# Performance work log

Hardware: AMD Instinct MI355X
Metric: run time of the kernel (lower is better)

The kernel has to match this reference:

```python
import jax, jax.numpy as jnp
import numpy as np

ONE_STEP = 14
EPS = 1e-5


def _bn(x, g, b):
    # training-mode batchnorm over the node/batch axis (biased variance)
    m = jnp.mean(x, axis=0)
    v = jnp.var(x, axis=0)
    return (x - m) * jax.lax.rsqrt(v + EPS) * g + b


def _gcn_conv(x, W, b, src, dst, dis):
    N = x.shape[0]
    h = x @ W
    norm = (dis[src] * dis[dst])[:, None]
    agg = jax.ops.segment_sum(h[src] * norm, dst, num_segments=N)
    agg = agg + (dis * dis)[:, None] * h  # self-loop contribution
    return agg + b


def setup_inputs() -> dict:
    key = jax.random.key(0)
    ks = jax.random.split(key, 16)
    N, F, E, NC = 114688, 512, 917504, 10
    x = jax.random.normal(ks[0], (N, F), jnp.float32)
    edge_index = jax.random.randint(ks[1], (2, E), 0, N, jnp.int32)

    def lin(k, i, o):
        return jax.random.normal(k, (i, o), jnp.float32) / np.sqrt(i).astype(np.float32)

    d = {"x": x, "edge_index": edge_index}
    dims = [(F, 128), (128, 256), (256, 64), (64, 32)]
    for li, (i, o) in enumerate(dims, 1):
        d[f"W{li}"] = lin(ks[1 + li], i, o)
        d[f"b{li}"] = jnp.zeros((o,), jnp.float32)
        d[f"bn{li}_g"] = jnp.ones((o,), jnp.float32)
        d[f"bn{li}_b"] = jnp.zeros((o,), jnp.float32)
    d["gW1"] = lin(ks[6], 32, 16); d["gb1"] = jnp.zeros((16,), jnp.float32)
    d["gbn1_g"] = jnp.ones((16,), jnp.float32); d["gbn1_b"] = jnp.zeros((16,), jnp.float32)
    d["gW2"] = lin(ks[7], 16, 1); d["gb2"] = jnp.zeros((1,), jnp.float32)
    d["gbn2_g"] = jnp.ones((1,), jnp.float32); d["gbn2_b"] = jnp.zeros((1,), jnp.float32)
    d["fcW"] = lin(ks[8], 32, NC); d["fcb"] = jnp.zeros((NC,), jnp.float32)
    return d


def reference(x, edge_index, W1, b1, bn1_g, bn1_b, W2, b2, bn2_g, bn2_b,
              W3, b3, bn3_g, bn3_b, W4, b4, bn4_g, bn4_b,
              gW1, gb1, gbn1_g, gbn1_b, gW2, gb2, gbn2_g, gbn2_b, fcW, fcb):
    N = x.shape[0]
    src, dst = edge_index[0], edge_index[1]
    # degree with self-loops (counted on dst, per PyG gcn_norm)
    deg = jax.ops.segment_sum(jnp.ones_like(dst, jnp.float32), dst, num_segments=N) + 1.0
    dis = jax.lax.rsqrt(deg)

    h = _bn(jax.nn.relu(_gcn_conv(x, W1, b1, src, dst, dis)), bn1_g, bn1_b)
    h = _bn(jax.nn.relu(_gcn_conv(h, W2, b2, src, dst, dis)), bn2_g, bn2_b)
    h = _bn(jax.nn.relu(_gcn_conv(h, W3, b3, src, dst, dis)), bn3_g, bn3_b)
    h = _bn(jax.nn.relu(_gcn_conv(h, W4, b4, src, dst, dis)), bn4_g, bn4_b)

    # gate network: Linear -> BN -> ReLU -> Linear -> BN -> ReLU
    g = jax.nn.relu(_bn(h @ gW1 + gb1, gbn1_g, gbn1_b))
    g = jax.nn.relu(_bn(g @ gW2 + gb2, gbn2_g, gbn2_b))[:, 0]  # [N]

    B = N // ONE_STEP
    batch = jnp.repeat(jnp.arange(B), ONE_STEP)
    # segment softmax over nodes of each graph
    m = jax.ops.segment_max(g, batch, num_segments=B)
    e = jnp.exp(g - m[batch])
    s = jax.ops.segment_sum(e, batch, num_segments=B)
    alpha = e / s[batch]
    pooled = jax.ops.segment_sum(alpha[:, None] * h, batch, num_segments=B)  # [B,32]

    # dropout is identity in eval mode
    logits = pooled @ fcW + fcb
    return jax.nn.softmax(logits, axis=1)
```

## Files before the change

kernel.cpp:

```cpp
#include <hip/hip_runtime.h>

#define NN 114688
#define NE 917504
#define NBATCH 8192
#define GSZ 14
#define NCLS 10
#define EPSB 1e-5f
#define NSCAN 112

typedef unsigned short u16;
typedef short bf16x8 __attribute__((ext_vector_type(8)));
typedef float f32x4 __attribute__((ext_vector_type(4)));
typedef _Float16 h8t __attribute__((ext_vector_type(8)));
typedef unsigned short u16x8 __attribute__((ext_vector_type(8)));

__device__ __forceinline__ float bf2f(u16 u) {
    union { unsigned int i; float f; } v; v.i = ((unsigned int)u) << 16; return v.f;
}
__device__ __forceinline__ u16 f2bf(float f) {
    union { float f; unsigned int i; } v; v.f = f;
    unsigned int i = v.i;
    unsigned int r = i + 0x7FFFu + ((i >> 16) & 1u);
    return (u16)(r >> 16);
}
__device__ __forceinline__ void splitbf(float y, u16& h, u16& l) {
    h = f2bf(y);
    l = f2bf(y - bf2f(h));
}

__global__ __launch_bounds__(256) void k_hist(const int* __restrict__ ei, int* __restrict__ counts) {
    int e = blockIdx.x * 256 + threadIdx.x;
    atomicAdd(&counts[ei[NE + e]], 1);
}

__global__ __launch_bounds__(256) void k_scan1(const int* __restrict__ counts, int* __restrict__ bsum) {
    __shared__ int red[256];
    int tid = threadIdx.x;
    int base = blockIdx.x * 1024 + tid * 4;
    int s = counts[base] + counts[base + 1] + counts[base + 2] + counts[base + 3];
    red[tid] = s; __syncthreads();
    for (int o = 128; o > 0; o >>= 1) {
        if (tid < o) red[tid] += red[tid + o];
        __syncthreads();
    }
    if (tid == 0) bsum[blockIdx.x] = red[0];
}

__global__ void k_scan2(int* bsum, int* offs) {
    if (threadIdx.x == 0) {
        int run = 0;
        for (int i = 0; i < NSCAN; i++) { int t = bsum[i]; bsum[i] = run; run += t; }
        offs[NN] = run;
    }
}

__global__ __launch_bounds__(256) void k_scan3(const int* __restrict__ counts, const int* __restrict__ bsum,
                                               int* __restrict__ offs) {
    __shared__ int ss[256];
    int tid = threadIdx.x;
    int base = blockIdx.x * 1024 + tid * 4;
    int v0 = counts[base], v1 = counts[base + 1], v2 = counts[base + 2], v3 = counts[base + 3];
    int ts = v0 + v1 + v2 + v3;
    ss[tid] = ts; __syncthreads();
    for (int o = 1; o < 256; o <<= 1) {
        int add = (tid >= o) ? ss[tid - o] : 0;
        __syncthreads();
        ss[tid] += add;
        __syncthreads();
    }
    int excl = ss[tid] - ts + bsum[blockIdx.x];
    offs[base] = excl;
    offs[base + 1] = excl + v0;
    offs[base + 2] = excl + v0 + v1;
    offs[base + 3] = excl + v0 + v1 + v2;
}

__global__ __launch_bounds__(256) void k_dis_cursor(const int* __restrict__ counts, const int* __restrict__ offs,
                                                    float* __restrict__ dis, int* __restrict__ cursor) {
    int n = blockIdx.x * 256 + threadIdx.x;
    dis[n] = rsqrtf((float)counts[n] + 1.0f);
    cursor[n] = offs[n];
}

__global__ __launch_bounds__(256) void k_scatter(const int* __restrict__ ei, int* __restrict__ cursor,
                                                 int* __restrict__ srcs, float* __restrict__ sd,
                                                 const float* __restrict__ dis, float* __restrict__ wsa) {
    int e = blockIdx.x * 256 + threadIdx.x;
    int d = ei[NE + e], s = ei[e];
    int p = atomicAdd(&cursor[d], 1);
    float w = dis[s];
    srcs[p] = s;
    sd[p] = w;
    atomicAdd(&wsa[d], w);
}

__global__ __launch_bounds__(256) void k_tsplit(const float* __restrict__ Wsrc,
                                                u16* __restrict__ Wh, u16* __restrict__ Wl,
                                                int K, int F) {
    int i = blockIdx.x * 256 + threadIdx.x;
    if (i < K * F) {
        int k = i / F, f = i % F;
        u16 h, l; splitbf(Wsrc[i], h, l);
        Wh[f * K + k] = h;
        Wl[f * K + k] = l;
    }
}

__global__ __launch_bounds__(256) void k_wsplit(const float* __restrict__ W, const float* __restrict__ sc,
                                                u16* __restrict__ Wh, u16* __restrict__ Wl,
                                                int K, int F) {
    int i = blockIdx.x * 256 + threadIdx.x;
    if (i < K * F) {
        int k = i / F, f = i % F;
        u16 h, l; splitbf(sc[k] * W[i], h, l);
        Wh[f * K + k] = h;
        Wl[f * K + k] = l;
    }
}

__global__ __launch_bounds__(256) void k_wc2(const float* __restrict__ W, const float* __restrict__ sh,
                                             float* __restrict__ c2, int K, int F) {
    int wv = (blockIdx.x * 256 + threadIdx.x) >> 6;
    int lane = threadIdx.x & 63;
    if (wv >= F) return;
    float acc = 0.f;
    for (int k = lane; k < K; k += 64) acc += sh[k] * W[k * F + wv];
#pragma unroll
    for (int o = 1; o < 64; o <<= 1) acc += __shfl_xor(acc, o);
    if (lane == 0) c2[wv] = acc;
}

template<int BM, int BN, int WCOLS, bool AFP32, bool C2, bool TEPI>
__global__ __launch_bounds__(256) void k_gemm(
    const float* __restrict__ Af, const u16* __restrict__ Ahi, const u16* __restrict__ Alo,
    const u16* __restrict__ Wh, const u16* __restrict__ Wl,
    _Float16* __restrict__ C, const int K, const int Fout, const float* __restrict__ c2,
    const float* __restrict__ bias, const float* __restrict__ wsa, const float* __restrict__ disv,
    u16* __restrict__ Thi, u16* __restrict__ Tlo, float* __restrict__ Sg, float* __restrict__ Qg)
{
    constexpr int AST = 40;
    __shared__ u16 Ah[BM][AST], Al[BM][AST];
    __shared__ u16 Bh[BN][AST], Bl[BN][AST];
    __shared__ float redS[TEPI ? BN : 1], redQ[TEPI ? BN : 1];

    const int tid = threadIdx.x;
    const int row0 = blockIdx.y * BM;
    const int col0 = blockIdx.x * BN;

    const int wave = tid >> 6, lane = tid & 63;
    const int mb = (wave / WCOLS) * 64;
    const int nb = (wave % WCOLS) * 64;
    const int lm = lane & 15;
    const int lk = (lane >> 4) * 8;
    const int cb = col0 + nb + lm;

    if constexpr (TEPI) {
        for (int i = tid; i < BN; i += 256) { redS[i] = 0.f; redQ[i] = 0.f; }
    }

    float c2v[4] = {0.f, 0.f, 0.f, 0.f};
    if constexpr (C2) {
#pragma unroll
        for (int ni = 0; ni < 4; ni++) c2v[ni] = c2[cb + ni * 16];
    }

    f32x4 acc[4][4];
#pragma unroll
    for (int i = 0; i < 4; i++)
#pragma unroll
        for (int j = 0; j < 4; j++)
#pragma unroll
            for (int r = 0; r < 4; r++) acc[i][j][r] = c2v[j];

    const int stg_r = tid >> 3;
    const int stg_c = (tid & 7) * 4;

    for (int k0 = 0; k0 < K; k0 += 32) {
        __syncthreads();
#pragma unroll
        for (int p = 0; p < BM / 32; p++) {
            const int r = p * 32 + stg_r;
            if constexpr (AFP32) {
                const float4 v = *(const float4*)(Af + (size_t)(row0 + r) * K + k0 + stg_c);
                float y[4] = {v.x, v.y, v.z, v.w};
                ushort4 hv, lv;
#pragma unroll
                for (int q = 0; q < 4; q++) splitbf(y[q], ((u16*)&hv)[q], ((u16*)&lv)[q]);
                *(ushort4*)&Ah[r][stg_c] = hv;
                *(ushort4*)&Al[r][stg_c] = lv;
            } else {
                *(ushort4*)&Ah[r][stg_c] = *(const ushort4*)(Ahi + (size_t)(row0 + r) * K + k0 + stg_c);
                *(ushort4*)&Al[r][stg_c] = *(const ushort4*)(Alo + (size_t)(row0 + r) * K + k0 + stg_c);
            }
        }
#pragma unroll
        for (int p = 0; p < BN / 32; p++) {
            const int n = p * 32 + stg_r;
            *(ushort4*)&Bh[n][stg_c] = *(const ushort4*)(Wh + (size_t)(col0 + n) * K + k0 + stg_c);
            *(ushort4*)&Bl[n][stg_c] = *(const ushort4*)(Wl + (size_t)(col0 + n) * K + k0 + stg_c);
        }
        __syncthreads();

        bf16x8 ah[4], al[4], bh[4], bl[4];
#pragma unroll
        for (int mi = 0; mi < 4; mi++) {
            ah[mi] = *(const bf16x8*)&Ah[mb + mi * 16 + lm][lk];
            al[mi] = *(const bf16x8*)&Al[mb + mi * 16 + lm][lk];
        }
#pragma unroll
        for (int ni = 0; ni < 4; ni++) {
            bh[ni] = *(const bf16x8*)&Bh[nb + ni * 16 + lm][lk];
            bl[ni] = *(const bf16x8*)&Bl[nb + ni * 16 + lm][lk];
        }
#pragma unroll
        for (int mi = 0; mi < 4; mi++)
#pragma unroll
            for (int ni = 0; ni < 4; ni++) {
                acc[mi][ni] = __builtin_amdgcn_mfma_f32_16x16x32_bf16(al[mi], bh[ni], acc[mi][ni], 0, 0, 0);
                acc[mi][ni] = __builtin_amdgcn_mfma_f32_16x16x32_bf16(ah[mi], bl[ni], acc[mi][ni], 0, 0, 0);
                acc[mi][ni] = __builtin_amdgcn_mfma_f32_16x16x32_bf16(ah[mi], bh[ni], acc[mi][ni], 0, 0, 0);
            }
    }

    const int rb = row0 + mb + (lane >> 4) * 4;
    if constexpr (TEPI) {
        float c2l[4], bl4[4];
#pragma unroll
        for (int ni = 0; ni < 4; ni++) { c2l[ni] = c2[cb + ni * 16]; bl4[ni] = bias[cb + ni * 16]; }
        float ws[4][4];
#pragma unroll
        for (int mi = 0; mi < 4; mi++)
#pragma unroll
            for (int r = 0; r < 4; r++) {
                const int row = rb + mi * 16 + r;
                const float d = disv[row];
                ws[mi][r] = d * wsa[row] + d * d;
            }
#pragma unroll
        for (int ni = 0; ni < 4; ni++) {
            float s = 0.f, q = 0.f;
#pragma unroll
            for (int mi = 0; mi < 4; mi++)
#pragma unroll
                for (int r = 0; r < 4; r++) {
                    float v = acc[mi][ni][r] + ws[mi][r] * c2l[ni] + bl4[ni];
                    v = fmaxf(v, 0.f);
                    s += v; q += v * v;
                    u16 hh, ll; splitbf(v, hh, ll);
                    const size_t idx = (size_t)(rb + mi * 16 + r) * Fout + cb + ni * 16;
                    Thi[idx] = hh;
                    Tlo[idx] = ll;
                }
            atomicAdd(&redS[nb + ni * 16 + lm], s);
            atomicAdd(&redQ[nb + ni * 16 + lm], q);
        }
        __syncthreads();
        for (int i = tid; i < BN; i += 256) {
            atomicAdd(&Sg[col0 + i], redS[i]);
            atomicAdd(&Qg[col0 + i], redQ[i]);
        }
    } else {
#pragma unroll
        for (int mi = 0; mi < 4; mi++)
#pragma unroll
            for (int ni = 0; ni < 4; ni++)
#pragma unroll
                for (int r = 0; r < 4; r++)
                    C[(size_t)(rb + mi * 16 + r) * Fout + cb + ni * 16] = (_Float16)acc[mi][ni][r];
    }
}

template<int CH, bool FP16OUT>
__global__ __launch_bounds__(256) void k_agg(
    const _Float16* __restrict__ h, u16* __restrict__ thi, u16* __restrict__ tlo,
    const float* __restrict__ bias,
    const int* __restrict__ off, const int* __restrict__ srcs, const float* __restrict__ sd,
    const float* __restrict__ dis, float* __restrict__ statS, float* __restrict__ statQ,
    _Float16* __restrict__ tf)
{
    constexpr int ECH = 16;
    constexpr int LPG = CH / ECH;
    constexpr int NSUB = 64 / LPG;
    __shared__ float redS[CH], redQ[CH];
    const int tid = threadIdx.x;
    for (int i = tid; i < CH; i += 256) { redS[i] = 0.f; redQ[i] = 0.f; }
    __syncthreads();

    const int lane = tid & 63;
    const int sub = lane / LPG;
    const int c = (lane % LPG) * ECH;
    const int wid = (blockIdx.x * 256 + tid) >> 6;
    const int nw = (gridDim.x * 256) >> 6;

    float bs[ECH], bq[ECH], bv[ECH];
#pragma unroll
    for (int v = 0; v < ECH; v++) { bs[v] = 0.f; bq[v] = 0.f; bv[v] = bias[c + v]; }

    for (int n = wid; n < NN; n += nw) {
        const int p0 = off[n], p1 = off[n + 1];
        float a[ECH];
#pragma unroll
        for (int v = 0; v < ECH; v++) a[v] = 0.f;

        int p = p0 + sub;
        int s = 0; float w = 0.f;
        if (p < p1) { s = srcs[p]; w = sd[p]; }
        while (p < p1) {
            const int pn = p + NSUB;
            int s2 = 0; float w2 = 0.f;
            if (pn < p1) { s2 = srcs[pn]; w2 = sd[pn]; }
            const _Float16* hr = h + (size_t)s * CH + c;
            h8t hv0 = *(const h8t*)hr;
            h8t hv1 = *(const h8t*)(hr + 8);
#pragma unroll
            for (int v = 0; v < 8; v++) { a[v] += w * (float)hv0[v]; a[v + 8] += w * (float)hv1[v]; }
            s = s2; w = w2; p = pn;
        }
#pragma unroll
        for (int o = LPG; o < 64; o <<= 1) {
#pragma unroll
            for (int v = 0; v < ECH; v++) a[v] += __shfl_xor(a[v], o);
        }
        if (sub == 0) {
            const float dn = dis[n];
            const float dn2 = dn * dn;
            const _Float16* hr = h + (size_t)n * CH + c;
            h8t hn0 = *(const h8t*)hr;
            h8t hn1 = *(const h8t*)(hr + 8);
            float o16[ECH];
#pragma unroll
            for (int v = 0; v < 8; v++) {
                o16[v] = fmaxf(dn * a[v] + dn2 * (float)hn0[v] + bv[v], 0.f);
                o16[v + 8] = fmaxf(dn * a[v + 8] + dn2 * (float)hn1[v] + bv[v + 8], 0.f);
            }
#pragma unroll
            for (int v = 0; v < ECH; v++) { bs[v] += o16[v]; bq[v] += o16[v] * o16[v]; }
            if constexpr (FP16OUT) {
                h8t o0, o1;
#pragma unroll
                for (int v = 0; v < 8; v++) { o0[v] = (_Float16)o16[v]; o1[v] = (_Float16)o16[v + 8]; }
                _Float16* tr = tf + (size_t)n * CH + c;
                *(h8t*)tr = o0; *(h8t*)(tr + 8) = o1;
            } else {
                u16x8 hv0, lv0, hv1, lv1;
#pragma unroll
                for (int v = 0; v < 8; v++) {
                    splitbf(o16[v], ((u16*)&hv0)[v], ((u16*)&lv0)[v]);
                    splitbf(o16[v + 8], ((u16*)&hv1)[v], ((u16*)&lv1)[v]);
                }
                u16* th = thi + (size_t)n * CH + c;
                u16* tl = tlo + (size_t)n * CH + c;
                *(u16x8*)th = hv0; *(u16x8*)(th + 8) = hv1;
                *(u16x8*)tl = lv0; *(u16x8*)(tl + 8) = lv1;
            }
        }
    }
    if (sub == 0) {
#pragma unroll
        for (int v = 0; v < ECH; v++) { atomicAdd(&redS[c + v], bs[v]); atomicAdd(&redQ[c + v], bq[v]); }
    }
    __syncthreads();
    for (int i = tid; i < CH; i += 256) { atomicAdd(&statS[i], redS[i]); atomicAdd(&statQ[i], redQ[i]); }
}

template<int CH>
__global__ __launch_bounds__(256) void k_agglin(
    const _Float16* __restrict__ t, u16* __restrict__ uhi, u16* __restrict__ ulo,
    const int* __restrict__ off, const int* __restrict__ srcs, const float* __restrict__ sd,
    const float* __restrict__ dis)
{
    constexpr int ECH = 16;
    constexpr int LPG = CH / ECH;
    constexpr int NSUB = 64 / LPG;
    const int tid = threadIdx.x;
    const int lane = tid & 63;
    const int sub = lane / LPG;
    const int c = (lane % LPG) * ECH;
    const int wid = (blockIdx.x * 256 + tid) >> 6;
    const int nw = (gridDim.x * 256) >> 6;

    for (int n = wid; n < NN; n += nw) {
        const int p0 = off[n], p1 = off[n + 1];
        float a[ECH];
#pragma unroll
        for (int v = 0; v < ECH; v++) a[v] = 0.f;

        int p = p0 + sub;
        int s = 0; float w = 0.f;
        if (p < p1) { s = srcs[p]; w = sd[p]; }
        while (p < p1) {
            const int pn = p + NSUB;
            int s2 = 0; float w2 = 0.f;
            if (pn < p1) { s2 = srcs[pn]; w2 = sd[pn]; }
            const _Float16* hr = t + (size_t)s * CH + c;
            h8t hv0 = *(const h8t*)hr;
            h8t hv1 = *(const h8t*)(hr + 8);
#pragma unroll
            for (int v = 0; v < 8; v++) { a[v] += w * (float)hv0[v]; a[v + 8] += w * (float)hv1[v]; }
            s = s2; w = w2; p = pn;
        }
#pragma unroll
        for (int o = LPG; o < 64; o <<= 1) {
#pragma unroll
            for (int v = 0; v < ECH; v++) a[v] += __shfl_xor(a[v], o);
        }
        if (sub == 0) {
            const float dn = dis[n];
            const float dn2 = dn * dn;
            const _Float16* hr = t + (size_t)n * CH + c;
            h8t hn0 = *(const h8t*)hr;
            h8t hn1 = *(const h8t*)(hr + 8);
            u16x8 hv0, lv0, hv1, lv1;
#pragma unroll
            for (int v = 0; v < 8; v++) {
                float o0 = dn * a[v] + dn2 * (float)hn0[v];
                float o1 = dn * a[v + 8] + dn2 * (float)hn1[v];
                splitbf(o0, ((u16*)&hv0)[v], ((u16*)&lv0)[v]);
                splitbf(o1, ((u16*)&hv1)[v], ((u16*)&lv1)[v]);
            }
            u16* th = uhi + (size_t)n * CH + c;
            u16* tl = ulo + (size_t)n * CH + c;
            *(u16x8*)th = hv0; *(u16x8*)(th + 8) = hv1;
            *(u16x8*)tl = lv0; *(u16x8*)(tl + 8) = lv1;
        }
    }
}

__global__ void k_bnpar(const float* __restrict__ S, const float* __restrict__ Q,
                        const float* __restrict__ g, const float* __restrict__ b,
                        float* __restrict__ sc, float* __restrict__ sh, int F) {
    int c = threadIdx.x;
    if (c >= F) return;
    const float invn = 1.0f / (float)NN;
    float mean = S[c] * invn;
    float var = Q[c] * invn - mean * mean;
    float s = g[c] * rsqrtf(fmaxf(var, 0.f) + EPSB);
    sc[c] = s;
    sh[c] = b[c] - mean * s;
}

template<int K, int F, bool BIAS, bool STATS>
__global__ __launch_bounds__(256) void k_smm(
    const u16* __restrict__ Ahi, const u16* __restrict__ Alo,
    const float* __restrict__ Wf, const float* __restrict__ bias,
    _Float16* __restrict__ C, const float* __restrict__ sc, const float* __restrict__ sh,
    float* __restrict__ Sg, float* __restrict__ Qg)
{
    __shared__ float Wl[K * F];
    __shared__ float scl[K], shl[K], bl[F];
    __shared__ float redS[F], redQ[F];
    const int tid = threadIdx.x;
    for (int i = tid; i < K * F; i += 256) Wl[i] = Wf[i];
    if (tid < K) { scl[tid] = sc[tid]; shl[tid] = sh[tid]; }
    if (tid < F) {
        bl[tid] = 0.f;
        if constexpr (BIAS) bl[tid] = bias[tid];
        if constexpr (STATS) { redS[tid] = 0.f; redQ[tid] = 0.f; }
    }
    __syncthreads();
    const int n = blockIdx.x * 256 + tid;
    float acc[F];
#pragma unroll
    for (int f = 0; f < F; f++) acc[f] = bl[f];
    const u16* ah = Ahi + (size_t)n * K;
    const u16* al = Alo + (size_t)n * K;
    for (int k = 0; k < K; k += 4) {
        ushort4 hv = *(const ushort4*)(ah + k);
        ushort4 lv = *(const ushort4*)(al + k);
        float y0 = (bf2f(hv.x) + bf2f(lv.x)) * scl[k] + shl[k];
        float y1 = (bf2f(hv.y) + bf2f(lv.y)) * scl[k + 1] + shl[k + 1];
        float y2 = (bf2f(hv.z) + bf2f(lv.z)) * scl[k + 2] + shl[k + 2];
        float y3 = (bf2f(hv.w) + bf2f(lv.w)) * scl[k + 3] + shl[k + 3];
#pragma unroll
        for (int f = 0; f < F; f += 4) {
            float4 w0 = *(const float4*)&Wl[k * F + f];
            float4 w1 = *(const float4*)&Wl[(k + 1) * F + f];
            float4 w2 = *(const float4*)&Wl[(k + 2) * F + f];
            float4 w3 = *(const float4*)&Wl[(k + 3) * F + f];
            acc[f + 0] += y0 * w0.x + y1 * w1.x + y2 * w2.x + y3 * w3.x;
            acc[f + 1] += y0 * w0.y + y1 * w1.y + y2 * w2.y + y3 * w3.y;
            acc[f + 2] += y0 * w0.z + y1 * w1.z + y2 * w2.z + y3 * w3.z;
            acc[f + 3] += y0 * w0.w + y1 * w1.w + y2 * w2.w + y3 * w3.w;
        }
    }
    _Float16* cr = C + (size_t)n * F;
#pragma unroll
    for (int f = 0; f < F; f++) cr[f] = (_Float16)acc[f];
    if constexpr (STATS) {
        float s[F], q[F];
#pragma unroll
        for (int f = 0; f < F; f++) { s[f] = acc[f]; q[f] = acc[f] * acc[f]; }
#pragma unroll
        for (int o = 1; o < 64; o <<= 1) {
#pragma unroll
            for (int f = 0; f < F; f++) { s[f] += __shfl_xor(s[f], o); q[f] += __shfl_xor(q[f], o); }
        }
        if ((tid & 63) == 0) {
#pragma unroll
            for (int f = 0; f < F; f++) { atomicAdd(&redS[f], s[f]); atomicAdd(&redQ[f], q[f]); }
        }
        __syncthreads();
        for (int i = tid; i < F; i += 256) { atomicAdd(&Sg[i], redS[i]); atomicAdd(&Qg[i], redQ[i]); }
    }
}

__global__ __launch_bounds__(256) void k_gate2(const _Float16* __restrict__ g1,
                                               const float* __restrict__ sc, const float* __restrict__ sh,
                                               const float* __restrict__ w2, const float* __restrict__ b2,
                                               float* __restrict__ g2,
                                               float* __restrict__ Sg, float* __restrict__ Qg) {
    __shared__ float wl[16], scl[16], shl[16], b2l[1];
    __shared__ float redSg[1], redQg[1];
    const int tid = threadIdx.x;
    if (tid < 16) { wl[tid] = w2[tid]; scl[tid] = sc[tid]; shl[tid] = sh[tid]; }
    if (tid == 0) { b2l[0] = b2[0]; redSg[0] = 0.f; redQg[0] = 0.f; }
    __syncthreads();
    const int n = blockIdx.x * 256 + tid;
    const _Float16* r = g1 + (size_t)n * 16;
    float acc = b2l[0];
#pragma unroll
    for (int k = 0; k < 16; k++) {
        float y = fmaxf((float)r[k] * scl[k] + shl[k], 0.f);
        acc += y * wl[k];
    }
    g2[n] = acc;
    float s = acc, q = acc * acc;
#pragma unroll
    for (int o = 1; o < 64; o <<= 1) { s += __shfl_xor(s, o); q += __shfl_xor(q, o); }
    if ((tid & 63) == 0) { atomicAdd(&redSg[0], s); atomicAdd(&redQg[0], q); }
    __syncthreads();
    if (tid == 0) { atomicAdd(&Sg[0], redSg[0]); atomicAdd(&Qg[0], redQg[0]); }
}

__global__ __launch_bounds__(256) void k_pool(const u16* __restrict__ t4hi, const u16* __restrict__ t4lo,
                                              const float* __restrict__ sc4, const float* __restrict__ sh4,
                                              const float* __restrict__ g2,
                                              const float* __restrict__ gsc2, const float* __restrict__ gsh2,
                                              const float* __restrict__ fcW, const float* __restrict__ fcb,
                                              float* __restrict__ out) {
    __shared__ float fw[32 * NCLS], fbl[NCLS], sc4l[32], sh4l[32];
    const int tid = threadIdx.x;
    for (int i = tid; i < 32 * NCLS; i += 256) fw[i] = fcW[i];
    if (tid < NCLS) fbl[tid] = fcb[tid];
    if (tid < 32) { sc4l[tid] = sc4[tid]; sh4l[tid] = sh4[tid]; }
    __syncthreads();
    const int b = blockIdx.x * 256 + tid;
    const float s2 = gsc2[0], h2 = gsh2[0];
    const int base = b * GSZ;

    float gv[GSZ];
    float m = -1e30f;
#pragma unroll
    for (int i = 0; i < GSZ; i++) {
        float v = fmaxf(g2[base + i] * s2 + h2, 0.f);
        gv[i] = v; m = fmaxf(m, v);
    }
    float ssum = 0.f;
#pragma unroll
    for (int i = 0; i < GSZ; i++) { float e = __expf(gv[i] - m); gv[i] = e; ssum += e; }
    const float inv = 1.0f / ssum;

    float pooled[32];
#pragma unroll
    for (int c = 0; c < 32; c++) pooled[c] = 0.f;
#pragma unroll
    for (int i = 0; i < GSZ; i++) {
        const float a = gv[i] * inv;
        const u16* th = t4hi + (size_t)(base + i) * 32;
        const u16* tl = t4lo + (size_t)(base + i) * 32;
#pragma unroll
        for (int c = 0; c < 32; c += 4) {
            ushort4 hv = *(const ushort4*)(th + c);
            ushort4 lv = *(const ushort4*)(tl + c);
            pooled[c + 0] += a * ((bf2f(hv.x) + bf2f(lv.x)) * sc4l[c + 0] + sh4l[c + 0]);
            pooled[c + 1] += a * ((bf2f(hv.y) + bf2f(lv.y)) * sc4l[c + 1] + sh4l[c + 1]);
            pooled[c + 2] += a * ((bf2f(hv.z) + bf2f(lv.z)) * sc4l[c + 2] + sh4l[c + 2]);
            pooled[c + 3] += a * ((bf2f(hv.w) + bf2f(lv.w)) * sc4l[c + 3] + sh4l[c + 3]);
        }
    }
    float lg[NCLS];
    float mx = -1e30f;
#pragma unroll
    for (int j = 0; j < NCLS; j++) {
        float a = fbl[j];
#pragma unroll
        for (int c = 0; c < 32; c++) a += pooled[c] * fw[c * NCLS + j];
        lg[j] = a; mx = fmaxf(mx, a);
    }
    float es = 0.f;
#pragma unroll
    for (int j = 0; j < NCLS; j++) { float e = __expf(lg[j] - mx); lg[j] = e; es += e; }
    const float iv = 1.0f / es;
#pragma unroll
    for (int j = 0; j < NCLS; j++) out[b * NCLS + j] = lg[j] * iv;
}

extern "C" void kernel_launch(void* const* d_in, const int* in_sizes, int n_in,
                              void* d_out, int out_size, void* d_ws, size_t ws_size,
                              hipStream_t stream) {
    (void)in_sizes; (void)n_in; (void)out_size; (void)ws_size;
    const float* x    = (const float*)d_in[0];
    const int*   ei   = (const int*)d_in[1];
    const float* W1   = (const float*)d_in[2];
    const float* b1   = (const float*)d_in[3];
    const float* bn1g = (const float*)d_in[4];
    const float* bn1b = (const float*)d_in[5];
    const float* W2   = (const float*)d_in[6];
    const float* b2   = (const float*)d_in[7];
    const float* bn2g = (const float*)d_in[8];
    const float* bn2b = (const float*)d_in[9];
    const float* W3   = (const float*)d_in[10];
    const float* b3   = (const float*)d_in[11];
    const float* bn3g = (const float*)d_in[12];
    const float* bn3b = (const float*)d_in[13];
    const float* W4   = (const float*)d_in[14];
    const float* b4   = (const float*)d_in[15];
    const float* bn4g = (const float*)d_in[16];
    const float* bn4b = (const float*)d_in[17];
    const float* gW1  = (const float*)d_in[18];
    const float* gb1  = (const float*)d_in[19];
    const float* gbn1g = (const float*)d_in[20];
    const float* gbn1b = (const float*)d_in[21];
    const float* gW2  = (const float*)d_in[22];
    const float* gb2  = (const float*)d_in[23];
    const float* gbn2g = (const float*)d_in[24];
    const float* gbn2b = (const float*)d_in[25];
    const float* fcW  = (const float*)d_in[26];
    const float* fcb  = (const float*)d_in[27];
    float* out = (float*)d_out;

    char* base = (char*)d_ws;
    size_t off_ = 0;
    auto carve = [&](size_t bytes) -> char* {
        char* p = base + off_;
        off_ = (off_ + bytes + 255) & ~(size_t)255;
        return p;
    };
    int*   counts = (int*)carve((size_t)NN * 4);
    float* stats  = (float*)carve(994 * 4);
    float* wsa    = (float*)carve((size_t)NN * 4);
    const size_t zero_bytes = off_;
    int*   offs   = (int*)carve((size_t)(NN + 1) * 4);
    int*   cursor = (int*)carve((size_t)NN * 4);
    int*   srcs   = (int*)carve((size_t)NE * 4);
    float* sd     = (float*)carve((size_t)NE * 4);
    float* dis    = (float*)carve((size_t)NN * 4);
    int*   bsum   = (int*)carve(NSCAN * 4);
    float* pars   = (float*)carve(994 * 4);
    u16*   Wt1h   = (u16*)carve(512 * 128 * 2);
    u16*   Wt1l   = (u16*)carve(512 * 128 * 2);
    u16*   Wt2h   = (u16*)carve(128 * 256 * 2);
    u16*   Wt2l   = (u16*)carve(128 * 256 * 2);
    u16*   Wt3h   = (u16*)carve(256 * 64 * 2);
    u16*   Wt3l   = (u16*)carve(256 * 64 * 2);
    float* c2_2   = (float*)carve(256 * 4);
    float* c2_3   = (float*)carve(64 * 4);
    float* g2raw  = (float*)carve((size_t)NN * 4);
    _Float16* P   = (_Float16*)carve((size_t)NN * 256 * 2);
    u16*   Qhi    = (u16*)carve((size_t)NN * 128 * 2);
    u16*   Qlo    = (u16*)carve((size_t)NN * 128 * 2);
    u16*   Rhi    = (u16*)carve((size_t)NN * 256 * 2);
    u16*   Rlo    = (u16*)carve((size_t)NN * 256 * 2);
    _Float16* T1f = P + (size_t)NN * 128;

    float* S1 = stats;      float* Q1s = S1 + 128;
    float* S2 = Q1s + 128;  float* Q2s = S2 + 256;
    float* S3 = Q2s + 256;  float* Q3s = S3 + 64;
    float* S4 = Q3s + 64;   float* Q4s = S4 + 32;
    float* gS1 = Q4s + 32;  float* gQ1 = gS1 + 16;
    float* gS2 = gQ1 + 16;  float* gQ2 = gS2 + 1;

    float* sc1 = pars;      float* sh1 = sc1 + 128;
    float* sc2 = sh1 + 128; float* sh2 = sc2 + 256;
    float* sc3 = sh2 + 256; float* sh3 = sc3 + 64;
    float* sc4 = sh3 + 64;  float* sh4 = sc4 + 32;
    float* gsc1 = sh4 + 32; float* gsh1 = gsc1 + 16;
    float* gsc2 = gsh1 + 16; float* gsh2 = gsc2 + 1;

    hipMemsetAsync(d_ws, 0, zero_bytes, stream);

    k_hist<<<NE / 256, 256, 0, stream>>>(ei, counts);
    k_scan1<<<NSCAN, 256, 0, stream>>>(counts, bsum);
    k_scan2<<<1, 64, 0, stream>>>(bsum, offs);
    k_scan3<<<NSCAN, 256, 0, stream>>>(counts, bsum, offs);
    k_dis_cursor<<<NN / 256, 256, 0, stream>>>(counts, offs, dis, cursor);
    k_scatter<<<NE / 256, 256, 0, stream>>>(ei, cursor, srcs, sd, dis, wsa);
    k_tsplit<<<(512 * 128 + 255) / 256, 256, 0, stream>>>(W1, Wt1h, Wt1l, 512, 128);

    k_gemm<128, 128, 2, true, false, false><<<dim3(1, NN / 128), 256, 0, stream>>>(
        x, nullptr, nullptr, Wt1h, Wt1l, P, 512, 128, nullptr,
        nullptr, nullptr, nullptr, nullptr, nullptr, nullptr, nullptr);
    k_agg<128, true><<<2048, 256, 0, stream>>>(P, nullptr, nullptr, b1, offs, srcs, sd, dis, S1, Q1s, T1f);
    k_bnpar<<<1, 256, 0, stream>>>(S1, Q1s, bn1g, bn1b, sc1, sh1, 128);

    k_agglin<128><<<2048, 256, 0, stream>>>(T1f, Qhi, Qlo, offs, srcs, sd, dis);
    k_wsplit<<<(128 * 256 + 255) / 256, 256, 0, stream>>>(W2, sc1, Wt2h, Wt2l, 128, 256);
    k_wc2<<<(256 * 64 + 255) / 256, 256, 0, stream>>>(W2, sh1, c2_2, 128, 256);
    k_gemm<128, 128, 2, false, false, true><<<dim3(2, NN / 128), 256, 0, stream>>>(
        nullptr, Qhi, Qlo, Wt2h, Wt2l, nullptr, 128, 256, c2_2,
        b2, wsa, dis, Rhi, Rlo, S2, Q2s);
    k_bnpar<<<1, 256, 0, stream>>>(S2, Q2s, bn2g, bn2b, sc2, sh2, 256);

    k_wsplit<<<(256 * 64 + 255) / 256, 256, 0, stream>>>(W3, sc2, Wt3h, Wt3l, 256, 64);
    k_wc2<<<(64 * 64 + 255) / 256, 256, 0, stream>>>(W3, sh2, c2_3, 256, 64);
    k_gemm<256, 64, 1, false, true, false><<<dim3(1, NN / 256), 256, 0, stream>>>(
        nullptr, Rhi, Rlo, Wt3h, Wt3l, P, 256, 64, c2_3,
        nullptr, nullptr, nullptr, nullptr, nullptr, nullptr, nullptr);
    k_agg<64, false><<<2048, 256, 0, stream>>>(P, Qhi, Qlo, b3, offs, srcs, sd, dis, S3, Q3s, nullptr);
    k_bnpar<<<1, 256, 0, stream>>>(S3, Q3s, bn3g, bn3b, sc3, sh3, 64);

    k_smm<64, 32, false, false><<<NN / 256, 256, 0, stream>>>(Qhi, Qlo, W4, nullptr, P, sc3, sh3,
                                                              nullptr, nullptr);
    k_agg<32, false><<<2048, 256, 0, stream>>>(P, Qhi, Qlo, b4, offs, srcs, sd, dis, S4, Q4s, nullptr);
    k_bnpar<<<1, 256, 0, stream>>>(S4, Q4s, bn4g, bn4b, sc4, sh4, 32);

    k_smm<32, 16, true, true><<<NN / 256, 256, 0, stream>>>(Qhi, Qlo, gW1, gb1, P, sc4, sh4, gS1, gQ1);
    k_bnpar<<<1, 256, 0, stream>>>(gS1, gQ1, gbn1g, gbn1b, gsc1, gsh1, 16);

    k_gate2<<<NN / 256, 256, 0, stream>>>(P, gsc1, gsh1, gW2, gb2, g2raw, gS2, gQ2);
    k_bnpar<<<1, 256, 0, stream>>>(gS2, gQ2, gbn2g, gbn2b, gsc2, gsh2, 1);

    k_pool<<<NBATCH / 256, 256, 0, stream>>>(Qhi, Qlo, sc4, sh4, g2raw, gsc2, gsh2, fcW, fcb, out);
}
```

Baseline: 1.145 ms.

## Assign one node per lane group in GCN aggregation instead of splitting edges

```diff
diff --git a/kernel.cpp b/kernel.cpp
--- a/kernel.cpp
+++ b/kernel.cpp
@@ -280,14 +280,15 @@
 {
     constexpr int ECH = 16;
     constexpr int LPG = CH / ECH;
-    constexpr int NSUB = 64 / LPG;
+    constexpr int G   = 64 / LPG;
+    constexpr int NB  = NN / G;
     __shared__ float redS[CH], redQ[CH];
     const int tid = threadIdx.x;
     for (int i = tid; i < CH; i += 256) { redS[i] = 0.f; redQ[i] = 0.f; }
     __syncthreads();
 
     const int lane = tid & 63;
-    const int sub = lane / LPG;
+    const int g = lane / LPG;
     const int c = (lane % LPG) * ECH;
     const int wid = (blockIdx.x * 256 + tid) >> 6;
     const int nw = (gridDim.x * 256) >> 6;
@@ -296,66 +297,64 @@
 #pragma unroll
     for (int v = 0; v < ECH; v++) { bs[v] = 0.f; bq[v] = 0.f; bv[v] = bias[c + v]; }
 
-    for (int n = wid; n < NN; n += nw) {
+    for (int b = wid; b < NB; b += nw) {
+        const int n = b * G + g;
         const int p0 = off[n], p1 = off[n + 1];
         float a[ECH];
 #pragma unroll
         for (int v = 0; v < ECH; v++) a[v] = 0.f;
 
-        int p = p0 + sub;
+        int p = p0;
         int s = 0; float w = 0.f;
         if (p < p1) { s = srcs[p]; w = sd[p]; }
         while (p < p1) {
-            const int pn = p + NSUB;
             int s2 = 0; float w2 = 0.f;
-            if (pn < p1) { s2 = srcs[pn]; w2 = sd[pn]; }
+            if (p + 1 < p1) { s2 = srcs[p + 1]; w2 = sd[p + 1]; }
             const _Float16* hr = h + (size_t)s * CH + c;
             h8t hv0 = *(const h8t*)hr;
             h8t hv1 = *(const h8t*)(hr + 8);
 #pragma unroll
             for (int v = 0; v < 8; v++) { a[v] += w * (float)hv0[v]; a[v + 8] += w * (float)hv1[v]; }
-            s = s2; w = w2; p = pn;
-        }
-#pragma unroll
-        for (int o = LPG; o < 64; o <<= 1) {
-#pragma unroll
-            for (int v = 0; v < ECH; v++) a[v] += __shfl_xor(a[v], o);
-        }
-        if (sub == 0) {
-            const float dn = dis[n];
-            const float dn2 = dn * dn;
-            const _Float16* hr = h + (size_t)n * CH + c;
-            h8t hn0 = *(const h8t*)hr;
-            h8t hn1 = *(const h8t*)(hr + 8);
-            float o16[ECH];
+            s = s2; w = w2; ++p;
+        }
+        const float dn = dis[n];
+        const float dn2 = dn * dn;
+        const _Float16* hr = h + (size_t)n * CH + c;
+        h8t hn0 = *(const h8t*)hr;
+        h8t hn1 = *(const h8t*)(hr + 8);
+        float o16[ECH];
+#pragma unroll
+        for (int v = 0; v < 8; v++) {
+            o16[v] = fmaxf(dn * a[v] + dn2 * (float)hn0[v] + bv[v], 0.f);
+            o16[v + 8] = fmaxf(dn * a[v + 8] + dn2 * (float)hn1[v] + bv[v + 8], 0.f);
+        }
+#pragma unroll
+        for (int v = 0; v < ECH; v++) { bs[v] += o16[v]; bq[v] += o16[v] * o16[v]; }
+        if constexpr (FP16OUT) {
+            h8t o0, o1;
+#pragma unroll
+            for (int v = 0; v < 8; v++) { o0[v] = (_Float16)o16[v]; o1[v] = (_Float16)o16[v + 8]; }
+            _Float16* tr = tf + (size_t)n * CH + c;
+            *(h8t*)tr = o0; *(h8t*)(tr + 8) = o1;
+        } else {
+            u16x8 hv0, lv0, hv1, lv1;
 #pragma unroll
             for (int v = 0; v < 8; v++) {
-                o16[v] = fmaxf(dn * a[v] + dn2 * (float)hn0[v] + bv[v], 0.f);
-                o16[v + 8] = fmaxf(dn * a[v + 8] + dn2 * (float)hn1[v] + bv[v + 8], 0.f);
+                splitbf(o16[v], ((u16*)&hv0)[v], ((u16*)&lv0)[v]);
+                splitbf(o16[v + 8], ((u16*)&hv1)[v], ((u16*)&lv1)[v]);
             }
-#pragma unroll
-            for (int v = 0; v < ECH; v++) { bs[v] += o16[v]; bq[v] += o16[v] * o16[v]; }
-            if constexpr (FP16OUT) {
-                h8t o0, o1;
-#pragma unroll
-                for (int v = 0; v < 8; v++) { o0[v] = (_Float16)o16[v]; o1[v] = (_Float16)o16[v + 8]; }
-                _Float16* tr = tf + (size_t)n * CH + c;
-                *(h8t*)tr = o0; *(h8t*)(tr + 8) = o1;
-            } else {
-                u16x8 hv0, lv0, hv1, lv1;
-#pragma unroll
-                for (int v = 0; v < 8; v++) {
-                    splitbf(o16[v], ((u16*)&hv0)[v], ((u16*)&lv0)[v]);
-                    splitbf(o16[v + 8], ((u16*)&hv1)[v], ((u16*)&lv1)[v]);
-                }
-                u16* th = thi + (size_t)n * CH + c;
-                u16* tl = tlo + (size_t)n * CH + c;
-                *(u16x8*)th = hv0; *(u16x8*)(th + 8) = hv1;
-                *(u16x8*)tl = lv0; *(u16x8*)(tl + 8) = lv1;
-            }
-        }
-    }
-    if (sub == 0) {
+            u16* th = thi + (size_t)n * CH + c;
+            u16* tl = tlo + (size_t)n * CH + c;
+            *(u16x8*)th = hv0; *(u16x8*)(th + 8) = hv1;
+            *(u16x8*)tl = lv0; *(u16x8*)(tl + 8) = lv1;
+        }
+    }
+#pragma unroll
+    for (int o = LPG; o < 64; o <<= 1) {
+#pragma unroll
+        for (int v = 0; v < ECH; v++) { bs[v] += __shfl_xor(bs[v], o); bq[v] += __shfl_xor(bq[v], o); }
+    }
+    if (g == 0) {
 #pragma unroll
         for (int v = 0; v < ECH; v++) { atomicAdd(&redS[c + v], bs[v]); atomicAdd(&redQ[c + v], bq[v]); }
     }
@@ -371,58 +370,52 @@
 {
     constexpr int ECH = 16;
     constexpr int LPG = CH / ECH;
-    constexpr int NSUB = 64 / LPG;
+    constexpr int G   = 64 / LPG;
+    constexpr int NB  = NN / G;
     const int tid = threadIdx.x;
     const int lane = tid & 63;
-    const int sub = lane / LPG;
+    const int g = lane / LPG;
     const int c = (lane % LPG) * ECH;
     const int wid = (blockIdx.x * 256 + tid) >> 6;
     const int nw = (gridDim.x * 256) >> 6;
 
-    for (int n = wid; n < NN; n += nw) {
+    for (int b = wid; b < NB; b += nw) {
+        const int n = b * G + g;
         const int p0 = off[n], p1 = off[n + 1];
         float a[ECH];
 #pragma unroll
         for (int v = 0; v < ECH; v++) a[v] = 0.f;
 
-        int p = p0 + sub;
+        int p = p0;
         int s = 0; float w = 0.f;
         if (p < p1) { s = srcs[p]; w = sd[p]; }
         while (p < p1) {
-            const int pn = p + NSUB;
             int s2 = 0; float w2 = 0.f;
-            if (pn < p1) { s2 = srcs[pn]; w2 = sd[pn]; }
+            if (p + 1 < p1) { s2 = srcs[p + 1]; w2 = sd[p + 1]; }
             const _Float16* hr = t + (size_t)s * CH + c;
             h8t hv0 = *(const h8t*)hr;
             h8t hv1 = *(const h8t*)(hr + 8);
 #pragma unroll
             for (int v = 0; v < 8; v++) { a[v] += w * (float)hv0[v]; a[v + 8] += w * (float)hv1[v]; }
-            s = s2; w = w2; p = pn;
-        }
-#pragma unroll
-        for (int o = LPG; o < 64; o <<= 1) {
-#pragma unroll
-            for (int v = 0; v < ECH; v++) a[v] += __shfl_xor(a[v], o);
-        }
-        if (sub == 0) {
-            const float dn = dis[n];
-            const float dn2 = dn * dn;
-            const _Float16* hr = t + (size_t)n * CH + c;
-            h8t hn0 = *(const h8t*)hr;
-            h8t hn1 = *(const h8t*)(hr + 8);
-            u16x8 hv0, lv0, hv1, lv1;
-#pragma unroll
-            for (int v = 0; v < 8; v++) {
-                float o0 = dn * a[v] + dn2 * (float)hn0[v];
-                float o1 = dn * a[v + 8] + dn2 * (float)hn1[v];
-                splitbf(o0, ((u16*)&hv0)[v], ((u16*)&lv0)[v]);
-                splitbf(o1, ((u16*)&hv1)[v], ((u16*)&lv1)[v]);
-            }
-            u16* th = uhi + (size_t)n * CH + c;
-            u16* tl = ulo + (size_t)n * CH + c;
-            *(u16x8*)th = hv0; *(u16x8*)(th + 8) = hv1;
-            *(u16x8*)tl = lv0; *(u16x8*)(tl + 8) = lv1;
-        }
+            s = s2; w = w2; ++p;
+        }
+        const float dn = dis[n];
+        const float dn2 = dn * dn;
+        const _Float16* hr = t + (size_t)n * CH + c;
+        h8t hn0 = *(const h8t*)hr;
+        h8t hn1 = *(const h8t*)(hr + 8);
+        u16x8 hv0, lv0, hv1, lv1;
+#pragma unroll
+        for (int v = 0; v < 8; v++) {
+            float o0 = dn * a[v] + dn2 * (float)hn0[v];
+            float o1 = dn * a[v + 8] + dn2 * (float)hn1[v];
+            splitbf(o0, ((u16*)&hv0)[v], ((u16*)&lv0)[v]);
+            splitbf(o1, ((u16*)&hv1)[v], ((u16*)&lv1)[v]);
+        }
+        u16* th = uhi + (size_t)n * CH + c;
+        u16* tl = ulo + (size_t)n * CH + c;
+        *(u16x8*)th = hv0; *(u16x8*)(th + 8) = hv1;
+        *(u16x8*)tl = lv0; *(u16x8*)(tl + 8) = lv1;
     }
 }
 
@@ -690,10 +683,10 @@
     k_gemm<128, 128, 2, true, false, false><<<dim3(1, NN / 128), 256, 0, stream>>>(
         x, nullptr, nullptr, Wt1h, Wt1l, P, 512, 128, nullptr,
         nullptr, nullptr, nullptr, nullptr, nullptr, nullptr, nullptr);
-    k_agg<128, true><<<2048, 256, 0, stream>>>(P, nullptr, nullptr, b1, offs, srcs, sd, dis, S1, Q1s, T1f);
+    k_agg<128, true><<<1792, 256, 0, stream>>>(P, nullptr, nullptr, b1, offs, srcs, sd, dis, S1, Q1s, T1f);
     k_bnpar<<<1, 256, 0, stream>>>(S1, Q1s, bn1g, bn1b, sc1, sh1, 128);
 
-    k_agglin<128><<<2048, 256, 0, stream>>>(T1f, Qhi, Qlo, offs, srcs, sd, dis);
+    k_agglin<128><<<1792, 256, 0, stream>>>(T1f, Qhi, Qlo, offs, srcs, sd, dis);
     k_wsplit<<<(128 * 256 + 255) / 256, 256, 0, stream>>>(W2, sc1, Wt2h, Wt2l, 128, 256);
     k_wc2<<<(256 * 64 + 255) / 256, 256, 0, stream>>>(W2, sh1, c2_2, 128, 256);
     k_gemm<128, 128, 2, false, false, true><<<dim3(2, NN / 128), 256, 0, stream>>>(
@@ -706,12 +699,12 @@
     k_gemm<256, 64, 1, false, true, false><<<dim3(1, NN / 256), 256, 0, stream>>>(
         nullptr, Rhi, Rlo, Wt3h, Wt3l, P, 256, 64, c2_3,
         nullptr, nullptr, nullptr, nullptr, nullptr, nullptr, nullptr);
-    k_agg<64, false><<<2048, 256, 0, stream>>>(P, Qhi, Qlo, b3, offs, srcs, sd, dis, S3, Q3s, nullptr);
+    k_agg<64, false><<<1792, 256, 0, stream>>>(P, Qhi, Qlo, b3, offs, srcs, sd, dis, S3, Q3s, nullptr);
     k_bnpar<<<1, 256, 0, stream>>>(S3, Q3s, bn3g, bn3b, sc3, sh3, 64);
 
     k_smm<64, 32, false, false><<<NN / 256, 256, 0, stream>>>(Qhi, Qlo, W4, nullptr, P, sc3, sh3,
                                                               nullptr, nullptr);
-    k_agg<32, false><<<2048, 256, 0, stream>>>(P, Qhi, Qlo, b4, offs, srcs, sd, dis, S4, Q4s, nullptr);
+    k_agg<32, false><<<896, 256, 0, stream>>>(P, Qhi, Qlo, b4, offs, srcs, sd, dis, S4, Q4s, nullptr);
     k_bnpar<<<1, 256, 0, stream>>>(S4, Q4s, bn4g, bn4b, sc4, sh4, 32);
 
     k_smm<32, 16, true, true><<<NN / 256, 256, 0, stream>>>(Qhi, Qlo, gW1, gb1, P, sc4, sh4, gS1, gQ1);
```

Result: faster. 974.9 us (-14.8%).
